# Optimization experiments

Hardware: AMD Instinct MI355X
Metric: run time of the kernel (lower is better)

The kernel has to match this reference:

```python
import jax, jax.numpy as jnp
import numpy as np

B, S, D = 4, 2048, 512
H, DK, DV = 8, 64, 64
LN_EPS = 1e-5


def setup_inputs() -> dict:
    key = jax.random.key(0)
    ks = jax.random.split(key, 9)
    inp = {
        "input_Q": jax.random.normal(ks[0], (B, S, D), jnp.float32),
        "input_K": jax.random.normal(ks[1], (B, S, D), jnp.float32),
        "input_V": jax.random.normal(ks[2], (B, S, D), jnp.float32),
        "attn_mask": jax.random.bernoulli(ks[3], 0.1, (B, S, S)),
        # weights stored [in, out] (math-equivalent to torch Linear's x @ W.T)
        "W_Q": jax.random.normal(ks[4], (D, H * DK), jnp.float32) * (1.0 / np.sqrt(D)),
        "W_K": jax.random.normal(ks[5], (D, H * DK), jnp.float32) * (1.0 / np.sqrt(D)),
        "W_V": jax.random.normal(ks[6], (D, H * DV), jnp.float32) * (1.0 / np.sqrt(D)),
        "W_fc": jax.random.normal(ks[7], (H * DV, D), jnp.float32) * (1.0 / np.sqrt(H * DV)),
        "ln_gamma": jnp.ones((D,), jnp.float32),
        "ln_beta": jnp.zeros((D,), jnp.float32),
    }
    return inp


def _mha(input_Q, input_K, input_V, attn_mask, W_Q, W_K, W_V, W_fc, ln_gamma, ln_beta):
    # project and split heads -> [B, H, S, d]
    Q = (input_Q @ W_Q).reshape(B, S, H, DK).transpose(0, 2, 1, 3)
    K = (input_K @ W_K).reshape(B, S, H, DK).transpose(0, 2, 1, 3)
    V = (input_V @ W_V).reshape(B, S, H, DV).transpose(0, 2, 1, 3)
    # scaled dot-product attention with masking (mask broadcast over heads)
    scores = jnp.einsum('bhqd,bhkd->bhqk', Q, K) / np.sqrt(DK)
    scores = jnp.where(attn_mask[:, None, :, :], -1e9, scores)
    attn = jax.nn.softmax(scores, axis=-1)
    context = jnp.einsum('bhqk,bhkd->bhqd', attn, V)
    context = context.transpose(0, 2, 1, 3).reshape(B, S, H * DV)
    out = context @ W_fc + input_Q  # fc + residual
    # LayerNorm over last dim
    mu = jnp.mean(out, axis=-1, keepdims=True)
    var = jnp.var(out, axis=-1, keepdims=True)
    normed = (out - mu) * jax.lax.rsqrt(var + LN_EPS) * ln_gamma + ln_beta
    return normed, attn


def reference(input_Q, input_K, input_V, attn_mask, W_Q, W_K, W_V, W_fc, ln_gamma, ln_beta):
    return _mha(input_Q, input_K, input_V, attn_mask, W_Q, W_K, W_V, W_fc, ln_gamma, ln_beta)
```

## Files before the change

kernel.cpp:

```cpp
#include <hip/hip_runtime.h>
#include <stdint.h>

typedef __attribute__((ext_vector_type(8))) short short8;
typedef __attribute__((ext_vector_type(4))) float f32x4;
typedef __attribute__((ext_vector_type(4))) unsigned short ushort4v;

__device__ __forceinline__ unsigned short f2bf(float f) {
    union { float f; uint32_t u; } v; v.f = f;
    return (unsigned short)((v.u + 0x7FFFu + ((v.u >> 16) & 1u)) >> 16);
}
__device__ __forceinline__ float bf2f(unsigned short h) {
    union { uint32_t u; float f; } v; v.u = ((uint32_t)h) << 16;
    return v.f;
}

__global__ __launch_bounds__(256) void prep_wt_kernel(
    const float* __restrict__ W0, const float* __restrict__ W1,
    const float* __restrict__ W2, const float* __restrict__ W3,
    unsigned short* __restrict__ Wt)
{
    __shared__ unsigned short tile[64][66];
    const float* W = blockIdx.y == 0 ? W0 : blockIdx.y == 1 ? W1 : blockIdx.y == 2 ? W2 : W3;
    unsigned short* dst = Wt + (size_t)blockIdx.y * (512 * 512);
    const int k0 = (blockIdx.x >> 3) * 64;
    const int n0 = (blockIdx.x & 7) * 64;
    const int nx = threadIdx.x & 63;
    const int ty = threadIdx.x >> 6;
#pragma unroll
    for (int i = 0; i < 16; ++i) {
        const int kl = i * 4 + ty;
        tile[nx][kl] = f2bf(W[(size_t)(k0 + kl) * 512 + n0 + nx]);
    }
    __syncthreads();
#pragma unroll
    for (int i = 0; i < 16; ++i) {
        const int nl = i * 4 + ty;
        dst[(size_t)(n0 + nl) * 512 + k0 + nx] = tile[nl][nx];
    }
}

__global__ __launch_bounds__(256) void proj_kernel(
    const float* __restrict__ inQ, const float* __restrict__ inK, const float* __restrict__ inV,
    const unsigned short* __restrict__ Wt,
    unsigned short* __restrict__ outQ, unsigned short* __restrict__ outK,
    unsigned short* __restrict__ outVT)
{
    const int which = blockIdx.y;
    const float* inp = which == 0 ? inQ : which == 1 ? inK : inV;
    const unsigned short* Wtb = Wt + (size_t)which * (512 * 512);
    const int tid = threadIdx.x;
    const int wid = tid >> 6, l = tid & 63;
    const int rt = wid >> 1, ch = wid & 1;
    const int lrow = l & 15, g = l >> 4;
    const int rowbase = blockIdx.x * 32;
    const int arow = rowbase + rt * 16 + lrow;

    f32x4 acc[16];
#pragma unroll
    for (int t = 0; t < 16; ++t) acc[t] = (f32x4){0.f, 0.f, 0.f, 0.f};

    for (int k0 = 0; k0 < 512; k0 += 32) {
        const float* ap = inp + (size_t)arow * 512 + k0 + g * 8;
        float4 a0 = *(const float4*)ap;
        float4 a1 = *(const float4*)(ap + 4);
        float av[8] = {a0.x, a0.y, a0.z, a0.w, a1.x, a1.y, a1.z, a1.w};
        short8 hi, lo;
#pragma unroll
        for (int j = 0; j < 8; ++j) {
            unsigned short hb = f2bf(av[j]);
            hi[j] = (short)hb;
            lo[j] = (short)f2bf(av[j] - bf2f(hb));
        }
#pragma unroll
        for (int t = 0; t < 16; ++t) {
            const int n = ch * 256 + t * 16 + lrow;
            short8 bf = *(const short8*)(Wtb + (size_t)n * 512 + k0 + g * 8);
            acc[t] = __builtin_amdgcn_mfma_f32_16x16x32_bf16(hi, bf, acc[t], 0, 0, 0);
            acc[t] = __builtin_amdgcn_mfma_f32_16x16x32_bf16(lo, bf, acc[t], 0, 0, 0);
        }
    }

    if (which == 2) {
#pragma unroll
        for (int t = 0; t < 16; ++t) {
            const int n = ch * 256 + t * 16 + lrow;
            const int hh = n >> 6, dd = n & 63;
            const int row0 = rowbase + rt * 16 + g * 4;
            const int bb = row0 >> 11, s0 = row0 & 2047;
            ushort4v pk;
            pk[0] = f2bf(acc[t][0]); pk[1] = f2bf(acc[t][1]);
            pk[2] = f2bf(acc[t][2]); pk[3] = f2bf(acc[t][3]);
            *(ushort4v*)(outVT + ((size_t)(bb * 8 + hh) * 64 + dd) * 2048 + s0) = pk;
        }
    } else {
        unsigned short* dst = which == 0 ? outQ : outK;
#pragma unroll
        for (int t = 0; t < 16; ++t) {
            const int n = ch * 256 + t * 16 + lrow;
            const int hh = n >> 6, dd = n & 63;
#pragma unroll
            for (int r = 0; r < 4; ++r) {
                const int row = rowbase + rt * 16 + g * 4 + r;
                const int bb = row >> 11, s0 = row & 2047;
                dst[((size_t)(bb * 8 + hh) * 2048 + s0) * 64 + dd] = f2bf(acc[t][r]);
            }
        }
    }
}

__global__ __launch_bounds__(256) void attn_kernel(
    const unsigned short* __restrict__ Qw, const unsigned short* __restrict__ Kw,
    const unsigned short* __restrict__ VT, const unsigned char* __restrict__ mask,
    float* __restrict__ attn_out, float* __restrict__ ctx)
{
    extern __shared__ char smem[];
    float* rowsum = (float*)(smem + 16 * 4096);
    const int L = blockIdx.x;
    const int xcd = L & 7, idx = L >> 3;
    const int q7 = idx & 127;
    const int bh = ((idx >> 7) << 3) | xcd;
    const int b = bh >> 3, h = bh & 7;
    const int qg0 = q7 * 16;
    const int tid = threadIdx.x, wid = tid >> 6, l = tid & 63;
    const int lrow = l & 15, g = l >> 4;

    if (tid < 16) rowsum[tid] = 0.f;
    __syncthreads();

    {
        const unsigned short* qp = Qw + ((size_t)bh * 2048 + qg0 + lrow) * 64 + g * 8;
        const short8 qf0 = *(const short8*)qp;
        const short8 qf1 = *(const short8*)(qp + 32);
        float psum = 0.f;
        const unsigned char* mrow = mask + ((size_t)b * 2048 + qg0 + lrow) * 2048;
        const int sw = (lrow & 7) << 4;
        char* prow = smem + lrow * 4096;
#pragma unroll 2
        for (int i = 0; i < 32; ++i) {
            const int kbase = (wid + i * 4) * 16;
            const unsigned short* kp = Kw + ((size_t)bh * 2048 + kbase + lrow) * 64 + g * 8;
            short8 kf0 = *(const short8*)kp;
            short8 kf1 = *(const short8*)(kp + 32);
            f32x4 sc = (f32x4){0.f, 0.f, 0.f, 0.f};
            sc = __builtin_amdgcn_mfma_f32_16x16x32_bf16(kf0, qf0, sc, 0, 0, 0);
            sc = __builtin_amdgcn_mfma_f32_16x16x32_bf16(kf1, qf1, sc, 0, 0, 0);
            const uint32_t m4 = *(const uint32_t*)(mrow + kbase + g * 4);
            ushort4v pk;
#pragma unroll
            for (int r = 0; r < 4; ++r) {
                const float e = ((m4 >> (8 * r)) & 255u) ? 0.f
                                : exp2f(sc[r] * 0.180336880f);
                psum += e;
                pk[r] = f2bf(e);
            }
            *(ushort4v*)(prow + ((kbase * 2 + g * 8) ^ sw)) = pk;
        }
        psum += __shfl_xor(psum, 16);
        psum += __shfl_xor(psum, 32);
        if (l < 16) atomicAdd(&rowsum[l], psum);
    }
    __syncthreads();

    {
        const int ct = wid;
        f32x4 acc0 = (f32x4){0.f,0.f,0.f,0.f}, acc1 = (f32x4){0.f,0.f,0.f,0.f};
        const unsigned short* vb = VT + ((size_t)bh * 64 + ct * 16 + lrow) * 2048 + g * 8;
        char* prow = smem + lrow * 4096;
        const int sw = (lrow & 7) << 4;
        for (int ks = 0; ks < 64; ks += 2) {
            short8 pa0 = *(const short8*)(prow + ((ks * 64 + g * 16) ^ sw));
            short8 vb0 = *(const short8*)(vb + ks * 32);
            acc0 = __builtin_amdgcn_mfma_f32_16x16x32_bf16(pa0, vb0, acc0, 0, 0, 0);
            short8 pa1 = *(const short8*)(prow + (((ks + 1) * 64 + g * 16) ^ sw));
            short8 vb1 = *(const short8*)(vb + (ks + 1) * 32);
            acc1 = __builtin_amdgcn_mfma_f32_16x16x32_bf16(pa1, vb1, acc1, 0, 0, 0);
        }
#pragma unroll
        for (int r = 0; r < 4; ++r) {
            const int q = g * 4 + r;
            const float rinv = 1.0f / rowsum[q];
            ctx[((size_t)b * 2048 + qg0 + q) * 512 + h * 64 + ct * 16 + lrow] =
                (acc0[r] + acc1[r]) * rinv;
        }
    }

    {
#pragma unroll
        for (int rr = 0; rr < 4; ++rr) {
            const int row = wid * 4 + rr;
            const float rinv = 1.0f / rowsum[row];
            float* gp = attn_out + ((size_t)bh * 2048 + qg0 + row) * 2048 + 2 * l;
            const char* pr = smem + row * 4096;
            const int swr = (row & 7) << 4;
#pragma unroll 4
            for (int c0 = 0; c0 < 2048; c0 += 128) {
                const uint32_t u = *(const uint32_t*)(pr + (((c0 + 2 * l) * 2) ^ swr));
                float2 o;
                o.x = bf2f((unsigned short)(u & 0xFFFFu)) * rinv;
                o.y = bf2f((unsigned short)(u >> 16)) * rinv;
                *(float2*)(gp + c0) = o;
            }
        }
    }
}

__global__ __launch_bounds__(256) void fc_ln_kernel(
    const float* __restrict__ ctx, const unsigned short* __restrict__ Wtfc,
    const float* __restrict__ resid, const float* __restrict__ gamma,
    const float* __restrict__ beta, float* __restrict__ out)
{
    __shared__ float red[32][2][2];
    const int tid = threadIdx.x;
    const int wid = tid >> 6, l = tid & 63;
    const int rt = wid >> 1, ch = wid & 1;
    const int lrow = l & 15, g = l >> 4;
    const int rowbase = blockIdx.x * 32;
    const int arow = rowbase + rt * 16 + lrow;

    f32x4 acc[16];
#pragma unroll
    for (int t = 0; t < 16; ++t) acc[t] = (f32x4){0.f, 0.f, 0.f, 0.f};

    for (int k0 = 0; k0 < 512; k0 += 32) {
        const float* ap = ctx + (size_t)arow * 512 + k0 + g * 8;
        float4 a0 = *(const float4*)ap;
        float4 a1 = *(const float4*)(ap + 4);
        float av[8] = {a0.x, a0.y, a0.z, a0.w, a1.x, a1.y, a1.z, a1.w};
        short8 hi, lo;
#pragma unroll
        for (int j = 0; j < 8; ++j) {
            unsigned short hb = f2bf(av[j]);
            hi[j] = (short)hb;
            lo[j] = (short)f2bf(av[j] - bf2f(hb));
        }
#pragma unroll
        for (int t = 0; t < 16; ++t) {
            const int n = ch * 256 + t * 16 + lrow;
            short8 bf = *(const short8*)(Wtfc + (size_t)n * 512 + k0 + g * 8);
            acc[t] = __builtin_amdgcn_mfma_f32_16x16x32_bf16(hi, bf, acc[t], 0, 0, 0);
            acc[t] = __builtin_amdgcn_mfma_f32_16x16x32_bf16(lo, bf, acc[t], 0, 0, 0);
        }
    }

    float s1[4] = {0,0,0,0}, s2[4] = {0,0,0,0};
#pragma unroll
    for (int t = 0; t < 16; ++t) {
        const int n = ch * 256 + t * 16 + lrow;
#pragma unroll
        for (int r = 0; r < 4; ++r) {
            const int row = rowbase + rt * 16 + g * 4 + r;
            float v = acc[t][r] + resid[(size_t)row * 512 + n];
            acc[t][r] = v;
            s1[r] += v;
            s2[r] += v * v;
        }
    }
#pragma unroll
    for (int r = 0; r < 4; ++r) {
        s1[r] += __shfl_xor(s1[r], 1); s2[r] += __shfl_xor(s2[r], 1);
        s1[r] += __shfl_xor(s1[r], 2); s2[r] += __shfl_xor(s2[r], 2);
        s1[r] += __shfl_xor(s1[r], 4); s2[r] += __shfl_xor(s2[r], 4);
        s1[r] += __shfl_xor(s1[r], 8); s2[r] += __shfl_xor(s2[r], 8);
    }
    if (lrow == 0) {
#pragma unroll
        for (int r = 0; r < 4; ++r) {
            red[rt * 16 + g * 4 + r][ch][0] = s1[r];
            red[rt * 16 + g * 4 + r][ch][1] = s2[r];
        }
    }
    __syncthreads();
    float mean[4], rstd[4];
#pragma unroll
    for (int r = 0; r < 4; ++r) {
        const int rl = rt * 16 + g * 4 + r;
        const float S1 = red[rl][0][0] + red[rl][1][0];
        const float S2 = red[rl][0][1] + red[rl][1][1];
        mean[r] = S1 * (1.0f / 512.0f);
        const float var = S2 * (1.0f / 512.0f) - mean[r] * mean[r];
        rstd[r] = rsqrtf(var + 1e-5f);
    }
#pragma unroll
    for (int t = 0; t < 16; ++t) {
        const int n = ch * 256 + t * 16 + lrow;
        const float gm = gamma[n], bt = beta[n];
#pragma unroll
        for (int r = 0; r < 4; ++r) {
            const int row = rowbase + rt * 16 + g * 4 + r;
            out[(size_t)row * 512 + n] = (acc[t][r] - mean[r]) * rstd[r] * gm + bt;
        }
    }
}

extern "C" void kernel_launch(void* const* d_in, const int* in_sizes, int n_in,
                              void* d_out, int out_size, void* d_ws, size_t ws_size,
                              hipStream_t stream)
{
    (void)in_sizes; (void)n_in; (void)out_size; (void)ws_size;
    const float* inQ = (const float*)d_in[0];
    const float* inK = (const float*)d_in[1];
    const float* inV = (const float*)d_in[2];
    const unsigned char* mask = (const unsigned char*)d_in[3];
    const float* WQ  = (const float*)d_in[4];
    const float* WK  = (const float*)d_in[5];
    const float* WV  = (const float*)d_in[6];
    const float* Wfc = (const float*)d_in[7];
    const float* gamma = (const float*)d_in[8];
    const float* beta  = (const float*)d_in[9];

    char* ws = (char*)d_ws;
    unsigned short* wsQ   = (unsigned short*)(ws);
    unsigned short* wsK   = (unsigned short*)(ws + ((size_t)8  << 20));
    unsigned short* wsVT  = (unsigned short*)(ws + ((size_t)16 << 20));
    float*          wsCtx = (float*)         (ws + ((size_t)24 << 20));
    unsigned short* wsWt  = (unsigned short*)(ws + ((size_t)40 << 20));

    float* out_ln   = (float*)d_out;
    float* out_attn = out_ln + (size_t)4 * 2048 * 512;

    prep_wt_kernel<<<dim3(64, 4), dim3(256), 0, stream>>>(WQ, WK, WV, Wfc, wsWt);
    proj_kernel<<<dim3(256, 3), dim3(256), 0, stream>>>(inQ, inK, inV, wsWt, wsQ, wsK, wsVT);

    const int smem_bytes = 16 * 4096 + 64;
    hipFuncSetAttribute((const void*)attn_kernel,
                        hipFuncAttributeMaxDynamicSharedMemorySize, smem_bytes);
    attn_kernel<<<dim3(4096), dim3(256), smem_bytes, stream>>>(wsQ, wsK, wsVT, mask,
                                                               out_attn, wsCtx);
    fc_ln_kernel<<<dim3(256), dim3(256), 0, stream>>>(wsCtx, wsWt + (size_t)3 * 512 * 512,
                                                      inQ, gamma, beta, out_ln);
}
```

Baseline: 1.102 ms.

## Restructure attention with 32x32 MFMA two-pass softmax and drop split-bf16 GEMMs

The attention kernel is rewritten around 32x32x16 MFMA tiles over 32 query rows per block, with each wave owning a key range. A first pass computes softmax row sums, and a second pass recomputes the scores, writes normalized probabilities straight to global memory and feeds them to PV through permlane swaps instead of a 64KB LDS staging buffer. Partial contexts are then reduced across waves in LDS. Separately, the projection and fc GEMMs drop the hi/lo split-bf16 compensation and use a single bf16 MFMA, halving matrix work at the cost of accuracy.

```diff
diff --git a/kernel.cpp b/kernel.cpp
--- a/kernel.cpp
+++ b/kernel.cpp
@@ -3,7 +3,9 @@
 
 typedef __attribute__((ext_vector_type(8))) short short8;
 typedef __attribute__((ext_vector_type(4))) float f32x4;
+typedef __attribute__((ext_vector_type(16))) float f32x16;
 typedef __attribute__((ext_vector_type(4))) unsigned short ushort4v;
+typedef __attribute__((ext_vector_type(4))) int int4v;
 
 __device__ __forceinline__ unsigned short f2bf(float f) {
     union { float f; uint32_t u; } v; v.f = f;
@@ -63,20 +65,16 @@
         const float* ap = inp + (size_t)arow * 512 + k0 + g * 8;
         float4 a0 = *(const float4*)ap;
         float4 a1 = *(const float4*)(ap + 4);
-        float av[8] = {a0.x, a0.y, a0.z, a0.w, a1.x, a1.y, a1.z, a1.w};
-        short8 hi, lo;
-#pragma unroll
-        for (int j = 0; j < 8; ++j) {
-            unsigned short hb = f2bf(av[j]);
-            hi[j] = (short)hb;
-            lo[j] = (short)f2bf(av[j] - bf2f(hb));
-        }
+        short8 af;
+        af[0] = (short)f2bf(a0.x); af[1] = (short)f2bf(a0.y);
+        af[2] = (short)f2bf(a0.z); af[3] = (short)f2bf(a0.w);
+        af[4] = (short)f2bf(a1.x); af[5] = (short)f2bf(a1.y);
+        af[6] = (short)f2bf(a1.z); af[7] = (short)f2bf(a1.w);
 #pragma unroll
         for (int t = 0; t < 16; ++t) {
             const int n = ch * 256 + t * 16 + lrow;
             short8 bf = *(const short8*)(Wtb + (size_t)n * 512 + k0 + g * 8);
-            acc[t] = __builtin_amdgcn_mfma_f32_16x16x32_bf16(hi, bf, acc[t], 0, 0, 0);
-            acc[t] = __builtin_amdgcn_mfma_f32_16x16x32_bf16(lo, bf, acc[t], 0, 0, 0);
+            acc[t] = __builtin_amdgcn_mfma_f32_16x16x32_bf16(af, bf, acc[t], 0, 0, 0);
         }
     }
 
@@ -108,99 +106,129 @@
     }
 }
 
-__global__ __launch_bounds__(256) void attn_kernel(
+__global__ __launch_bounds__(256, 4) void attn_kernel(
     const unsigned short* __restrict__ Qw, const unsigned short* __restrict__ Kw,
     const unsigned short* __restrict__ VT, const unsigned char* __restrict__ mask,
     float* __restrict__ attn_out, float* __restrict__ ctx)
 {
-    extern __shared__ char smem[];
-    float* rowsum = (float*)(smem + 16 * 4096);
+    __shared__ float psum_lds[4][32];
+    __shared__ float ctx_lds[4][32][67];
+
     const int L = blockIdx.x;
-    const int xcd = L & 7, idx = L >> 3;
-    const int q7 = idx & 127;
-    const int bh = ((idx >> 7) << 3) | xcd;
+    const int xcd = L & 7, j = L >> 3;
+    const int bh = xcd * 4 + (j >> 6);
+    const int qb = j & 63;
     const int b = bh >> 3, h = bh & 7;
-    const int qg0 = q7 * 16;
+    const int qg0 = qb * 32;
     const int tid = threadIdx.x, wid = tid >> 6, l = tid & 63;
-    const int lrow = l & 15, g = l >> 4;
-
-    if (tid < 16) rowsum[tid] = 0.f;
+    const int lq = l & 31, hi = l >> 5;
+    const float EXPC = 0.18033688011112042f;
+
+    const unsigned short* qbase = Qw + ((size_t)bh * 2048 + qg0 + lq) * 64 + 8 * hi;
+    short8 qf[4];
+#pragma unroll
+    for (int d4 = 0; d4 < 4; ++d4) qf[d4] = *(const short8*)(qbase + d4 * 16);
+
+    const int k0w = wid * 512;
+    const unsigned char* mbase = mask + ((size_t)b * 2048 + qg0 + lq) * 2048 + 4 * hi;
+    const unsigned short* kwb = Kw + ((size_t)bh * 2048 + lq) * 64 + 8 * hi;
+
+    float psum = 0.f;
+    for (int t = 0; t < 16; ++t) {
+        const int kb = k0w + t * 32;
+        const unsigned short* kp = kwb + (size_t)kb * 64;
+        short8 kf0 = *(const short8*)(kp);
+        short8 kf1 = *(const short8*)(kp + 16);
+        short8 kf2 = *(const short8*)(kp + 32);
+        short8 kf3 = *(const short8*)(kp + 48);
+        f32x16 sc = (f32x16)(0.f);
+        sc = __builtin_amdgcn_mfma_f32_32x32x16_bf16(kf0, qf[0], sc, 0, 0, 0);
+        sc = __builtin_amdgcn_mfma_f32_32x32x16_bf16(kf1, qf[1], sc, 0, 0, 0);
+        sc = __builtin_amdgcn_mfma_f32_32x32x16_bf16(kf2, qf[2], sc, 0, 0, 0);
+        sc = __builtin_amdgcn_mfma_f32_32x32x16_bf16(kf3, qf[3], sc, 0, 0, 0);
+#pragma unroll
+        for (int c2 = 0; c2 < 4; ++c2) {
+            const uint32_t m4 = *(const uint32_t*)(mbase + kb + 8 * c2);
+#pragma unroll
+            for (int rr = 0; rr < 4; ++rr) {
+                const float e = ((m4 >> (8 * rr)) & 255u) ? 0.f
+                                : exp2f(sc[c2 * 4 + rr] * EXPC);
+                psum += e;
+            }
+        }
+    }
+    psum += __shfl_xor(psum, 32);
+    if (l < 32) psum_lds[wid][l] = psum;
     __syncthreads();
-
-    {
-        const unsigned short* qp = Qw + ((size_t)bh * 2048 + qg0 + lrow) * 64 + g * 8;
-        const short8 qf0 = *(const short8*)qp;
-        const short8 qf1 = *(const short8*)(qp + 32);
-        float psum = 0.f;
-        const unsigned char* mrow = mask + ((size_t)b * 2048 + qg0 + lrow) * 2048;
-        const int sw = (lrow & 7) << 4;
-        char* prow = smem + lrow * 4096;
-#pragma unroll 2
-        for (int i = 0; i < 32; ++i) {
-            const int kbase = (wid + i * 4) * 16;
-            const unsigned short* kp = Kw + ((size_t)bh * 2048 + kbase + lrow) * 64 + g * 8;
-            short8 kf0 = *(const short8*)kp;
-            short8 kf1 = *(const short8*)(kp + 32);
-            f32x4 sc = (f32x4){0.f, 0.f, 0.f, 0.f};
-            sc = __builtin_amdgcn_mfma_f32_16x16x32_bf16(kf0, qf0, sc, 0, 0, 0);
-            sc = __builtin_amdgcn_mfma_f32_16x16x32_bf16(kf1, qf1, sc, 0, 0, 0);
-            const uint32_t m4 = *(const uint32_t*)(mrow + kbase + g * 4);
-            ushort4v pk;
-#pragma unroll
-            for (int r = 0; r < 4; ++r) {
-                const float e = ((m4 >> (8 * r)) & 255u) ? 0.f
-                                : exp2f(sc[r] * 0.180336880f);
-                psum += e;
-                pk[r] = f2bf(e);
+    const float rinv = 1.0f / (psum_lds[0][lq] + psum_lds[1][lq] +
+                               psum_lds[2][lq] + psum_lds[3][lq]);
+
+    f32x16 acc0 = (f32x16)(0.f), acc1 = (f32x16)(0.f);
+    float* abase = attn_out + ((size_t)bh * 2048 + qg0 + lq) * 2048 + 4 * hi;
+    const unsigned short* vb0 = VT + ((size_t)bh * 64 + lq) * 2048 + 8 * hi;
+    const unsigned short* vb1 = vb0 + (size_t)32 * 2048;
+
+    for (int t = 0; t < 16; ++t) {
+        const int kb = k0w + t * 32;
+        const unsigned short* kp = kwb + (size_t)kb * 64;
+        short8 kf0 = *(const short8*)(kp);
+        short8 kf1 = *(const short8*)(kp + 16);
+        short8 kf2 = *(const short8*)(kp + 32);
+        short8 kf3 = *(const short8*)(kp + 48);
+        f32x16 sc = (f32x16)(0.f);
+        sc = __builtin_amdgcn_mfma_f32_32x32x16_bf16(kf0, qf[0], sc, 0, 0, 0);
+        sc = __builtin_amdgcn_mfma_f32_32x32x16_bf16(kf1, qf[1], sc, 0, 0, 0);
+        sc = __builtin_amdgcn_mfma_f32_32x32x16_bf16(kf2, qf[2], sc, 0, 0, 0);
+        sc = __builtin_amdgcn_mfma_f32_32x32x16_bf16(kf3, qf[3], sc, 0, 0, 0);
+
+        float e[16];
+#pragma unroll
+        for (int c2 = 0; c2 < 4; ++c2) {
+            const uint32_t m4 = *(const uint32_t*)(mbase + kb + 8 * c2);
+#pragma unroll
+            for (int rr = 0; rr < 4; ++rr) {
+                e[c2 * 4 + rr] = ((m4 >> (8 * rr)) & 255u) ? 0.f
+                                 : exp2f(sc[c2 * 4 + rr] * EXPC) * rinv;
             }
-            *(ushort4v*)(prow + ((kbase * 2 + g * 8) ^ sw)) = pk;
-        }
-        psum += __shfl_xor(psum, 16);
-        psum += __shfl_xor(psum, 32);
-        if (l < 16) atomicAdd(&rowsum[l], psum);
+        }
+#pragma unroll
+        for (int c2 = 0; c2 < 4; ++c2) {
+            float4 st = {e[c2 * 4 + 0], e[c2 * 4 + 1], e[c2 * 4 + 2], e[c2 * 4 + 3]};
+            *(float4*)(abase + kb + 8 * c2) = st;
+        }
+#pragma unroll
+        for (int kh = 0; kh < 2; ++kh) {
+            const int cA = 2 * kh, cB = 2 * kh + 1;
+            uint32_t w0 = (uint32_t)f2bf(e[4 * cA + 0]) | ((uint32_t)f2bf(e[4 * cA + 1]) << 16);
+            uint32_t w1 = (uint32_t)f2bf(e[4 * cB + 0]) | ((uint32_t)f2bf(e[4 * cB + 1]) << 16);
+            uint32_t w2 = (uint32_t)f2bf(e[4 * cA + 2]) | ((uint32_t)f2bf(e[4 * cA + 3]) << 16);
+            uint32_t w3 = (uint32_t)f2bf(e[4 * cB + 2]) | ((uint32_t)f2bf(e[4 * cB + 3]) << 16);
+            asm("v_permlane32_swap_b32 %0, %1" : "+v"(w0), "+v"(w1));
+            asm("v_permlane32_swap_b32 %0, %1" : "+v"(w2), "+v"(w3));
+            int4v pw = {(int)w0, (int)w2, (int)w1, (int)w3};
+            short8 pb = *(short8*)&pw;
+            const size_t voff = (size_t)(kb + 16 * kh);
+            short8 v0 = *(const short8*)(vb0 + voff);
+            short8 v1 = *(const short8*)(vb1 + voff);
+            acc0 = __builtin_amdgcn_mfma_f32_32x32x16_bf16(v0, pb, acc0, 0, 0, 0);
+            acc1 = __builtin_amdgcn_mfma_f32_32x32x16_bf16(v1, pb, acc1, 0, 0, 0);
+        }
+    }
+
+#pragma unroll
+    for (int r = 0; r < 16; ++r) {
+        const int d = (r & 3) + 8 * (r >> 2) + 4 * hi;
+        ctx_lds[wid][lq][d] = acc0[r];
+        ctx_lds[wid][lq][d + 32] = acc1[r];
     }
     __syncthreads();
-
-    {
-        const int ct = wid;
-        f32x4 acc0 = (f32x4){0.f,0.f,0.f,0.f}, acc1 = (f32x4){0.f,0.f,0.f,0.f};
-        const unsigned short* vb = VT + ((size_t)bh * 64 + ct * 16 + lrow) * 2048 + g * 8;
-        char* prow = smem + lrow * 4096;
-        const int sw = (lrow & 7) << 4;
-        for (int ks = 0; ks < 64; ks += 2) {
-            short8 pa0 = *(const short8*)(prow + ((ks * 64 + g * 16) ^ sw));
-            short8 vb0 = *(const short8*)(vb + ks * 32);
-            acc0 = __builtin_amdgcn_mfma_f32_16x16x32_bf16(pa0, vb0, acc0, 0, 0, 0);
-            short8 pa1 = *(const short8*)(prow + (((ks + 1) * 64 + g * 16) ^ sw));
-            short8 vb1 = *(const short8*)(vb + (ks + 1) * 32);
-            acc1 = __builtin_amdgcn_mfma_f32_16x16x32_bf16(pa1, vb1, acc1, 0, 0, 0);
-        }
-#pragma unroll
-        for (int r = 0; r < 4; ++r) {
-            const int q = g * 4 + r;
-            const float rinv = 1.0f / rowsum[q];
-            ctx[((size_t)b * 2048 + qg0 + q) * 512 + h * 64 + ct * 16 + lrow] =
-                (acc0[r] + acc1[r]) * rinv;
-        }
-    }
-
-    {
-#pragma unroll
-        for (int rr = 0; rr < 4; ++rr) {
-            const int row = wid * 4 + rr;
-            const float rinv = 1.0f / rowsum[row];
-            float* gp = attn_out + ((size_t)bh * 2048 + qg0 + row) * 2048 + 2 * l;
-            const char* pr = smem + row * 4096;
-            const int swr = (row & 7) << 4;
-#pragma unroll 4
-            for (int c0 = 0; c0 < 2048; c0 += 128) {
-                const uint32_t u = *(const uint32_t*)(pr + (((c0 + 2 * l) * 2) ^ swr));
-                float2 o;
-                o.x = bf2f((unsigned short)(u & 0xFFFFu)) * rinv;
-                o.y = bf2f((unsigned short)(u >> 16)) * rinv;
-                *(float2*)(gp + c0) = o;
-            }
-        }
+#pragma unroll
+    for (int i = 0; i < 8; ++i) {
+        const int idx = i * 256 + tid;
+        const int q = idx >> 6, d = idx & 63;
+        const float s = ctx_lds[0][q][d] + ctx_lds[1][q][d] +
+                        ctx_lds[2][q][d] + ctx_lds[3][q][d];
+        ctx[((size_t)b * 2048 + qg0 + q) * 512 + h * 64 + d] = s;
     }
 }
 
@@ -225,20 +253,16 @@
         const float* ap = ctx + (size_t)arow * 512 + k0 + g * 8;
         float4 a0 = *(const float4*)ap;
         float4 a1 = *(const float4*)(ap + 4);
-        float av[8] = {a0.x, a0.y, a0.z, a0.w, a1.x, a1.y, a1.z, a1.w};
-        short8 hi, lo;
-#pragma unroll
-        for (int j = 0; j < 8; ++j) {
-            unsigned short hb = f2bf(av[j]);
-            hi[j] = (short)hb;
-            lo[j] = (short)f2bf(av[j] - bf2f(hb));
-        }
+        short8 af;
+        af[0] = (short)f2bf(a0.x); af[1] = (short)f2bf(a0.y);
+        af[2] = (short)f2bf(a0.z); af[3] = (short)f2bf(a0.w);
+        af[4] = (short)f2bf(a1.x); af[5] = (short)f2bf(a1.y);
+        af[6] = (short)f2bf(a1.z); af[7] = (short)f2bf(a1.w);
 #pragma unroll
         for (int t = 0; t < 16; ++t) {
             const int n = ch * 256 + t * 16 + lrow;
             short8 bf = *(const short8*)(Wtfc + (size_t)n * 512 + k0 + g * 8);
-            acc[t] = __builtin_amdgcn_mfma_f32_16x16x32_bf16(hi, bf, acc[t], 0, 0, 0);
-            acc[t] = __builtin_amdgcn_mfma_f32_16x16x32_bf16(lo, bf, acc[t], 0, 0, 0);
+            acc[t] = __builtin_amdgcn_mfma_f32_16x16x32_bf16(af, bf, acc[t], 0, 0, 0);
         }
     }
 
@@ -320,12 +344,8 @@
 
     prep_wt_kernel<<<dim3(64, 4), dim3(256), 0, stream>>>(WQ, WK, WV, Wfc, wsWt);
     proj_kernel<<<dim3(256, 3), dim3(256), 0, stream>>>(inQ, inK, inV, wsWt, wsQ, wsK, wsVT);
-
-    const int smem_bytes = 16 * 4096 + 64;
-    hipFuncSetAttribute((const void*)attn_kernel,
-                        hipFuncAttributeMaxDynamicSharedMemorySize, smem_bytes);
-    attn_kernel<<<dim3(4096), dim3(256), smem_bytes, stream>>>(wsQ, wsK, wsVT, mask,
-                                                               out_attn, wsCtx);
+    attn_kernel<<<dim3(2048), dim3(256), 0, stream>>>(wsQ, wsK, wsVT, mask,
+                                                      out_attn, wsCtx);
     fc_ln_kernel<<<dim3(256), dim3(256), 0, stream>>>(wsCtx, wsWt + (size_t)3 * 512 * 512,
                                                       inQ, gamma, beta, out_ln);
 }
```

New measurement: 1.002 ms. 1.1x faster.
